# Kernel tuning notes

Hardware: AMD Instinct MI355X
Metric: run time of the kernel (lower is better)

Reference implementation:

```python
import jax, jax.numpy as jnp
import numpy as np

B, S, IN_F, OUT_F = 4, 2048, 4096, 4096

def setup_inputs() -> dict:
    key = jax.random.key(0)
    k1, k2, k3 = jax.random.split(key, 3)
    # int8 activations and weights (symmetric range)
    x = jax.random.randint(k1, (B, S, IN_F), -128, 128, dtype=jnp.int32).astype(jnp.int8)
    weight_q = jax.random.randint(k2, (OUT_F, IN_F), -128, 128, dtype=jnp.int32).astype(jnp.int8)
    scale_x = jnp.float32(0.05)   # activation quant scale
    scale_w = jnp.float32(0.02)   # weight quant scale (scalar, per-tensor)
    scale_y = jax.random.uniform(k3, (OUT_F,), minval=0.5, maxval=2.0, dtype=jnp.float32)  # per-output-row scale
    return {"x": x, "weight_q": weight_q, "scale_x": scale_x, "scale_w": scale_w, "scale_y": scale_y}

def reference(x, weight_q, scale_x, scale_w, scale_y):
    # int8 GEMM with int32 accumulation: [B,S,IN] @ [OUT,IN]^T -> [B,S,OUT]
    acc = jax.lax.dot_general(x, weight_q, ((((2,), (1,)), ((), ()))),
                              preferred_element_type=jnp.int32)
    # fused requantization scale: scale_x * scale_w / scale_y  -> [OUT]
    requant_scale = (scale_x * scale_w / scale_y).astype(jnp.float32)
    out_f = acc.astype(jnp.float32) * requant_scale  # broadcast over last dim
    out_q = jnp.clip(jnp.round(out_f), -128, 127).astype(jnp.int8)
    return out_q, scale_y
```

## Files before the change

kernel.cpp:

```cpp
#include <hip/hip_runtime.h>
#include <cstdint>


#define MDIM 8192
#define NDIM 4096
#define KDIM 4096
#define BM 256
#define BN 256
#define NH 64

typedef int v4i __attribute__((ext_vector_type(4)));

__device__ __forceinline__ uint32_t pack4(int a, int b, int c, int d) {
  return (uint32_t)(a & 0xFF) | ((uint32_t)(b & 0xFF) << 8) |
         ((uint32_t)(c & 0xFF) << 16) | ((uint32_t)(d & 0xFF) << 24);
}

__global__ __launch_bounds__(256) void pack_kernel(
    const int* __restrict__ x32, const int* __restrict__ w32,
    const float* __restrict__ sy, uint8_t* __restrict__ x8f,
    uint8_t* __restrict__ w8f, float* __restrict__ tail) {
  const int t = blockIdx.x * 256 + threadIdx.x;
  if (t < NDIM) tail[t] = sy[t];
  const int NXC = (MDIM / 16) * KDIM;
  const int NWC = (NDIM / 16) * KDIM;
  if (t >= NXC + NWC) return;
  const int* src;
  uint8_t* dst;
  int chunk;
  if (t < NXC) {
    chunk = t;
    src = x32;
    dst = x8f;
  } else {
    chunk = t - NXC;
    src = w32;
    dst = w8f;
  }
  const int lpos = chunk & 63;
  const int rf = (chunk >> 6) & 15;
  const int h = (chunk >> 10) & 63;
  const int mb = chunk >> 16;
  const int kl = lpos >> 4, fr = lpos & 15;
  const int r = mb * 256 + rf * 16 + fr;
  const int k0 = h * 64 + kl * 16;
  const int* s = src + (size_t)r * KDIM + k0;
  v4i a0 = *(const v4i*)(s + 0);
  v4i a1 = *(const v4i*)(s + 4);
  v4i a2 = *(const v4i*)(s + 8);
  v4i a3 = *(const v4i*)(s + 12);
  v4i o;
  o[0] = (int)pack4(a0[0], a0[1], a0[2], a0[3]);
  o[1] = (int)pack4(a1[0], a1[1], a1[2], a1[3]);
  o[2] = (int)pack4(a2[0], a2[1], a2[2], a2[3]);
  o[3] = (int)pack4(a3[0], a3[1], a3[2], a3[3]);
  *(v4i*)(dst + (size_t)chunk * 16) = o;
}

__global__ __launch_bounds__(256, 1) void gemm_kernel(
    const uint8_t* __restrict__ A8, const uint8_t* __restrict__ B8,
    const float* __restrict__ sxp, const float* __restrict__ swp,
    const float* __restrict__ syp, float* __restrict__ out) {
  __shared__ __align__(16) uint8_t lds[131072];

  const int tid = threadIdx.x;
  const int lane = tid & 63;
  const int wave = tid >> 6;

  const int wg = ((int)blockIdx.x % 8) * 64 + (int)blockIdx.x / 8;
  const int mb = wg >> 4;
  const int nb = wg & 15;

  const int wm2 = wave >> 1;
  const int wn2 = wave & 1;

  const uint8_t* Asrc = A8 + ((size_t)mb << 20) + ((size_t)wm2 << 13);
  const uint8_t* Bsrc = B8 + ((size_t)nb << 20) + ((size_t)wn2 << 13);

  uint8_t* wlds = lds + wave * 32768;
  const uint32_t lane16 = (uint32_t)lane * 16;

  v4i acc[8][8];
#pragma unroll
  for (int i = 0; i < 8; i++)
#pragma unroll
    for (int j = 0; j < 8; j++) acc[i][j] = (v4i){0, 0, 0, 0};

  auto gload = [&](const uint8_t* src, uint8_t* ldst) {
    __builtin_amdgcn_global_load_lds(
        (const __attribute__((address_space(1))) void*)src,
        (__attribute__((address_space(3))) void*)ldst, 16, 0, 0);
  };
  auto stage = [&](int h) {
    const uint32_t rb = (uint32_t)(h & 1) * 16384u;
    const uint8_t* sa = Asrc + ((size_t)h << 14) + lane16;
    const uint8_t* sb = Bsrc + ((size_t)h << 14) + lane16;
    uint8_t* la = wlds + rb + lane16;
#pragma unroll
    for (int r = 0; r < 8; ++r) {
      gload(sa + r * 1024, la + r * 1024);
      gload(sb + r * 1024, la + 8192 + r * 1024);
    }
  };

  stage(0);

  for (int h = 0; h < NH; ++h) {
    if (h + 1 < NH) {
      stage(h + 1);
      asm volatile("s_waitcnt vmcnt(16)" ::: "memory");
    } else {
      asm volatile("s_waitcnt vmcnt(0)" ::: "memory");
    }
    const uint8_t* LA = wlds + (uint32_t)(h & 1) * 16384u;
    const uint8_t* LB = LA + 8192;

    v4i af[8], bf[8];
#pragma unroll
    for (int i = 0; i < 8; i++)
      af[i] = *(const v4i*)(LA + (i << 10) + lane16);
#pragma unroll
    for (int j = 0; j < 8; j++)
      bf[j] = *(const v4i*)(LB + (j << 10) + lane16);

#pragma unroll
    for (int i = 0; i < 8; i++)
#pragma unroll
      for (int j = 0; j < 8; j++)
        acc[i][j] =
            __builtin_amdgcn_mfma_i32_16x16x64_i8(af[i], bf[j], acc[i][j], 0, 0, 0);
  }

  const float s = sxp[0] * swp[0];
  const int kl = lane >> 4;
  const int fr = lane & 15;
  const int wrow = mb * 256 + wm2 * 128;
  const int wcol = nb * 256 + wn2 * 128;
#pragma unroll
  for (int j = 0; j < 8; j++) {
    const int col = wcol + j * 16 + fr;
    const float rs = s / syp[col];
#pragma unroll
    for (int i = 0; i < 8; i++) {
      const int row0 = wrow + i * 16 + kl * 4;
#pragma unroll
      for (int r = 0; r < 4; r++) {
        float v = rintf((float)acc[i][j][r] * rs);
        v = fminf(127.f, fmaxf(-128.f, v));
        out[(size_t)(row0 + r) * NDIM + col] = v;
      }
    }
  }
}

extern "C" void kernel_launch(void* const* d_in, const int* in_sizes, int n_in,
                              void* d_out, int out_size, void* d_ws, size_t ws_size,
                              hipStream_t stream) {
  const int* x32 = (const int*)d_in[0];
  const int* w32 = (const int*)d_in[1];
  const float* sx = (const float*)d_in[2];
  const float* sw = (const float*)d_in[3];
  const float* sy = (const float*)d_in[4];
  float* out = (float*)d_out;
  float* tail = out + (size_t)MDIM * NDIM;

  uint8_t* x8f = (uint8_t*)d_ws;
  uint8_t* w8f = x8f + (size_t)MDIM * KDIM;

  const int total = (MDIM / 16) * KDIM + (NDIM / 16) * KDIM;
  pack_kernel<<<total / 256, 256, 0, stream>>>(x32, w32, sy, x8f, w8f, tail);

  const int nblocks = (MDIM / BM) * (NDIM / BN);
  gemm_kernel<<<nblocks, 256, 0, stream>>>(x8f, w8f, sx, sw, sy, out);
}
```

Before: 207.2 us.

## Load GEMM fragments directly from global into registers, dropping LDS staging

Each wave no longer stages its A/B fragments through LDS via global_load_lds. It now loads them straight from global memory into two register buffers and double-buffers across K steps, with no LDS use at all. This removes the LDS round trip and the 128KB LDS allocation. In exchange it adds register pressure (32 extra v4i on top of 256 accumulator VGPRs), which could cause spills. The compiler now decides the waitcnt placement, so latency hiding may get worse.

Result: faster. 185.8 us (-10.3%).

```diff
diff --git a/kernel.cpp b/kernel.cpp
--- a/kernel.cpp
+++ b/kernel.cpp
@@ -61,8 +61,6 @@
     const uint8_t* __restrict__ A8, const uint8_t* __restrict__ B8,
     const float* __restrict__ sxp, const float* __restrict__ swp,
     const float* __restrict__ syp, float* __restrict__ out) {
-  __shared__ __align__(16) uint8_t lds[131072];
-
   const int tid = threadIdx.x;
   const int lane = tid & 63;
   const int wave = tid >> 6;
@@ -74,11 +72,10 @@
   const int wm2 = wave >> 1;
   const int wn2 = wave & 1;
 
-  const uint8_t* Asrc = A8 + ((size_t)mb << 20) + ((size_t)wm2 << 13);
-  const uint8_t* Bsrc = B8 + ((size_t)nb << 20) + ((size_t)wn2 << 13);
-
-  uint8_t* wlds = lds + wave * 32768;
-  const uint32_t lane16 = (uint32_t)lane * 16;
+  const uint8_t* Asrc =
+      A8 + ((size_t)mb << 20) + ((size_t)wm2 << 13) + (size_t)lane * 16;
+  const uint8_t* Bsrc =
+      B8 + ((size_t)nb << 20) + ((size_t)wn2 << 13) + (size_t)lane * 16;
 
   v4i acc[8][8];
 #pragma unroll
@@ -86,50 +83,36 @@
 #pragma unroll
     for (int j = 0; j < 8; j++) acc[i][j] = (v4i){0, 0, 0, 0};
 
-  auto gload = [&](const uint8_t* src, uint8_t* ldst) {
-    __builtin_amdgcn_global_load_lds(
-        (const __attribute__((address_space(1))) void*)src,
-        (__attribute__((address_space(3))) void*)ldst, 16, 0, 0);
+  v4i a0[8], b0[8], a1[8], b1[8];
+
+  auto load = [&](v4i(&a)[8], v4i(&b)[8], int h) {
+    const uint8_t* pa = Asrc + ((size_t)h << 14);
+    const uint8_t* pb = Bsrc + ((size_t)h << 14);
+#pragma unroll
+    for (int i = 0; i < 8; i++) a[i] = *(const v4i*)(pa + (i << 10));
+#pragma unroll
+    for (int j = 0; j < 8; j++) b[j] = *(const v4i*)(pb + (j << 10));
   };
-  auto stage = [&](int h) {
-    const uint32_t rb = (uint32_t)(h & 1) * 16384u;
-    const uint8_t* sa = Asrc + ((size_t)h << 14) + lane16;
-    const uint8_t* sb = Bsrc + ((size_t)h << 14) + lane16;
-    uint8_t* la = wlds + rb + lane16;
-#pragma unroll
-    for (int r = 0; r < 8; ++r) {
-      gload(sa + r * 1024, la + r * 1024);
-      gload(sb + r * 1024, la + 8192 + r * 1024);
-    }
-  };
-
-  stage(0);
-
-  for (int h = 0; h < NH; ++h) {
-    if (h + 1 < NH) {
-      stage(h + 1);
-      asm volatile("s_waitcnt vmcnt(16)" ::: "memory");
-    } else {
-      asm volatile("s_waitcnt vmcnt(0)" ::: "memory");
-    }
-    const uint8_t* LA = wlds + (uint32_t)(h & 1) * 16384u;
-    const uint8_t* LB = LA + 8192;
-
-    v4i af[8], bf[8];
-#pragma unroll
-    for (int i = 0; i < 8; i++)
-      af[i] = *(const v4i*)(LA + (i << 10) + lane16);
-#pragma unroll
-    for (int j = 0; j < 8; j++)
-      bf[j] = *(const v4i*)(LB + (j << 10) + lane16);
-
+  auto mfma = [&](v4i(&a)[8], v4i(&b)[8]) {
 #pragma unroll
     for (int i = 0; i < 8; i++)
 #pragma unroll
       for (int j = 0; j < 8; j++)
         acc[i][j] =
-            __builtin_amdgcn_mfma_i32_16x16x64_i8(af[i], bf[j], acc[i][j], 0, 0, 0);
+            __builtin_amdgcn_mfma_i32_16x16x64_i8(a[i], b[j], acc[i][j], 0, 0, 0);
+  };
+
+  load(a0, b0, 0);
+  load(a1, b1, 1);
+
+  for (int h = 0; h < NH - 2; h += 2) {
+    mfma(a0, b0);
+    load(a0, b0, h + 2);
+    mfma(a1, b1);
+    load(a1, b1, h + 3);
   }
+  mfma(a0, b0);
+  mfma(a1, b1);
 
   const float s = sxp[0] * swp[0];
   const int kl = lane >> 4;
```

## Shrink GEMM tiles to 128x128 with shared cooperative LDS staging and barriers

Applied to the files above, without the earlier changes.

Tiles drop from 256x256 to 128x128, and the pack layout changes to match. Instead of each wave privately loading its own A/B slices into LDS, all four waves now cooperatively load one shared 16KB-per-stage tile and synchronise with a block barrier. The launch bound is raised to 3 blocks per CU so occupancy and latency hiding improve. In exchange, each block reuses less data per load and pays a full vmcnt(0) wait plus a barrier every k-step.

Result: no change. 210.8 us (+1.8%).

```diff
diff --git a/kernel.cpp b/kernel.cpp
--- a/kernel.cpp
+++ b/kernel.cpp
@@ -5,11 +5,19 @@
 #define MDIM 8192
 #define NDIM 4096
 #define KDIM 4096
-#define BM 256
-#define BN 256
+#define BM 128
+#define BN 128
 #define NH 64
 
 typedef int v4i __attribute__((ext_vector_type(4)));
+
+#define FENCE() asm volatile("" ::: "memory")
+#define BARX()                    \
+  do {                            \
+    FENCE();                      \
+    __builtin_amdgcn_s_barrier(); \
+    FENCE();                      \
+  } while (0)
 
 __device__ __forceinline__ uint32_t pack4(int a, int b, int c, int d) {
   return (uint32_t)(a & 0xFF) | ((uint32_t)(b & 0xFF) << 8) |
@@ -38,11 +46,11 @@
     dst = w8f;
   }
   const int lpos = chunk & 63;
-  const int rf = (chunk >> 6) & 15;
-  const int h = (chunk >> 10) & 63;
-  const int mb = chunk >> 16;
+  const int rf = (chunk >> 6) & 7;
+  const int h = (chunk >> 9) & 63;
+  const int mb = chunk >> 15;
   const int kl = lpos >> 4, fr = lpos & 15;
-  const int r = mb * 256 + rf * 16 + fr;
+  const int r = mb * 128 + rf * 16 + fr;
   const int k0 = h * 64 + kl * 16;
   const int* s = src + (size_t)r * KDIM + k0;
   v4i a0 = *(const v4i*)(s + 0);
@@ -57,76 +65,71 @@
   *(v4i*)(dst + (size_t)chunk * 16) = o;
 }
 
-__global__ __launch_bounds__(256, 1) void gemm_kernel(
+__global__ __launch_bounds__(256, 3) void gemm_kernel(
     const uint8_t* __restrict__ A8, const uint8_t* __restrict__ B8,
     const float* __restrict__ sxp, const float* __restrict__ swp,
     const float* __restrict__ syp, float* __restrict__ out) {
-  __shared__ __align__(16) uint8_t lds[131072];
+  __shared__ __align__(16) uint8_t lds[32768];
 
   const int tid = threadIdx.x;
   const int lane = tid & 63;
   const int wave = tid >> 6;
 
-  const int wg = ((int)blockIdx.x % 8) * 64 + (int)blockIdx.x / 8;
-  const int mb = wg >> 4;
-  const int nb = wg & 15;
+  const int wg = ((int)blockIdx.x & 7) * 256 + ((int)blockIdx.x >> 3);
+  const int mb = wg >> 5;
+  const int nb = wg & 31;
 
   const int wm2 = wave >> 1;
   const int wn2 = wave & 1;
 
-  const uint8_t* Asrc = A8 + ((size_t)mb << 20) + ((size_t)wm2 << 13);
-  const uint8_t* Bsrc = B8 + ((size_t)nb << 20) + ((size_t)wn2 << 13);
+  const uint8_t* Abase = A8 + ((size_t)mb << 19);
+  const uint8_t* Bbase = B8 + ((size_t)nb << 19);
 
-  uint8_t* wlds = lds + wave * 32768;
+  const uint32_t tid16 = (uint32_t)tid * 16;
   const uint32_t lane16 = (uint32_t)lane * 16;
+  const uint32_t aoff = (uint32_t)(wm2 * 4) << 10;
+  const uint32_t boff = 8192u + ((uint32_t)(wn2 * 4) << 10);
 
-  v4i acc[8][8];
+  v4i acc[4][4];
 #pragma unroll
-  for (int i = 0; i < 8; i++)
+  for (int i = 0; i < 4; i++)
 #pragma unroll
-    for (int j = 0; j < 8; j++) acc[i][j] = (v4i){0, 0, 0, 0};
+    for (int j = 0; j < 4; j++) acc[i][j] = (v4i){0, 0, 0, 0};
 
-  auto gload = [&](const uint8_t* src, uint8_t* ldst) {
+  auto gload = [&](const uint8_t* src, uint32_t ldsoff) {
     __builtin_amdgcn_global_load_lds(
         (const __attribute__((address_space(1))) void*)src,
-        (__attribute__((address_space(3))) void*)ldst, 16, 0, 0);
+        (__attribute__((address_space(3))) void*)(lds + ldsoff), 16, 0, 0);
   };
   auto stage = [&](int h) {
-    const uint32_t rb = (uint32_t)(h & 1) * 16384u;
-    const uint8_t* sa = Asrc + ((size_t)h << 14) + lane16;
-    const uint8_t* sb = Bsrc + ((size_t)h << 14) + lane16;
-    uint8_t* la = wlds + rb + lane16;
-#pragma unroll
-    for (int r = 0; r < 8; ++r) {
-      gload(sa + r * 1024, la + r * 1024);
-      gload(sb + r * 1024, la + 8192 + r * 1024);
-    }
+    const uint32_t lb = (uint32_t)(h & 1) * 16384u;
+    const uint8_t* sa = Abase + ((size_t)h << 13) + tid16;
+    const uint8_t* sb = Bbase + ((size_t)h << 13) + tid16;
+    gload(sa, lb + tid16);
+    gload(sa + 4096, lb + 4096u + tid16);
+    gload(sb, lb + 8192u + tid16);
+    gload(sb + 4096, lb + 12288u + tid16);
   };
 
   stage(0);
 
   for (int h = 0; h < NH; ++h) {
-    if (h + 1 < NH) {
-      stage(h + 1);
-      asm volatile("s_waitcnt vmcnt(16)" ::: "memory");
-    } else {
-      asm volatile("s_waitcnt vmcnt(0)" ::: "memory");
-    }
-    const uint8_t* LA = wlds + (uint32_t)(h & 1) * 16384u;
-    const uint8_t* LB = LA + 8192;
+    asm volatile("s_waitcnt vmcnt(0)" ::: "memory");
+    BARX();
+    if (h + 1 < NH) stage(h + 1);
 
-    v4i af[8], bf[8];
+    const uint8_t* L = lds + (uint32_t)(h & 1) * 16384u;
+    v4i af[4], bf[4];
 #pragma unroll
-    for (int i = 0; i < 8; i++)
-      af[i] = *(const v4i*)(LA + (i << 10) + lane16);
+    for (int i = 0; i < 4; i++)
+      af[i] = *(const v4i*)(L + aoff + (i << 10) + lane16);
 #pragma unroll
-    for (int j = 0; j < 8; j++)
-      bf[j] = *(const v4i*)(LB + (j << 10) + lane16);
-
+    for (int j = 0; j < 4; j++)
+      bf[j] = *(const v4i*)(L + boff + (j << 10) + lane16);
 #pragma unroll
-    for (int i = 0; i < 8; i++)
+    for (int i = 0; i < 4; i++)
 #pragma unroll
-      for (int j = 0; j < 8; j++)
+      for (int j = 0; j < 4; j++)
         acc[i][j] =
             __builtin_amdgcn_mfma_i32_16x16x64_i8(af[i], bf[j], acc[i][j], 0, 0, 0);
   }
@@ -134,14 +137,14 @@
   const float s = sxp[0] * swp[0];
   const int kl = lane >> 4;
   const int fr = lane & 15;
-  const int wrow = mb * 256 + wm2 * 128;
-  const int wcol = nb * 256 + wn2 * 128;
+  const int wrow = mb * 128 + wm2 * 64;
+  const int wcol = nb * 128 + wn2 * 64;
 #pragma unroll
-  for (int j = 0; j < 8; j++) {
+  for (int j = 0; j < 4; j++) {
     const int col = wcol + j * 16 + fr;
     const float rs = s / syp[col];
 #pragma unroll
-    for (int i = 0; i < 8; i++) {
+    for (int i = 0; i < 4; i++) {
       const int row0 = wrow + i * 16 + kl * 4;
 #pragma unroll
       for (int r = 0; r < 4; r++) {
```
